# Kernel tuning notes

Measured on AMD Instinct MI355X. Metric: run time of the kernel, lower is better.

The kernel has to match this reference:

```python
import jax, jax.numpy as jnp
import numpy as np

B, T, C = 8, 1024, 768
NH = 12
HD = C // NH  # 64


def setup_inputs() -> dict:
    key = jax.random.key(0)
    k1, k2, k3 = jax.random.split(key, 3)
    x = jax.random.normal(k1, (B, T, C), dtype=jnp.float32)
    w_attn = jax.random.normal(k2, (C, 3 * C), dtype=jnp.float32) * 0.02
    b_attn = jnp.zeros((3 * C,), dtype=jnp.float32)
    w_proj = jax.random.normal(k3, (C, C), dtype=jnp.float32) * 0.02
    b_proj = jnp.zeros((C,), dtype=jnp.float32)
    return {"x": x, "w_attn": w_attn, "b_attn": b_attn, "w_proj": w_proj, "b_proj": b_proj}


def reference(x, w_attn, b_attn, w_proj, b_proj):
    Bb, Tt, Cc = x.shape
    qkv = x @ w_attn + b_attn  # [B,T,3C]
    q, k, v = jnp.split(qkv, [Cc, 2 * Cc], axis=-1)
    # [B, NH, T, HD]
    q = q.reshape(Bb, Tt, NH, HD).swapaxes(1, 2)
    k = k.reshape(Bb, Tt, NH, HD).swapaxes(1, 2)
    v = v.reshape(Bb, Tt, NH, HD).swapaxes(1, 2)
    scale = 1.0 / jnp.sqrt(jnp.asarray(HD, dtype=x.dtype))
    att = jnp.einsum("bhqd,bhkd->bhqk", q, k) * scale  # [B,NH,T,T]
    causal = jnp.tril(jnp.ones((Tt, Tt), dtype=bool))[None, None]
    att = jnp.where(causal, att, jnp.asarray(-jnp.inf, dtype=att.dtype))
    att = jax.nn.softmax(att, axis=-1)
    y = jnp.einsum("bhqk,bhkd->bhqd", att, v)  # [B,NH,T,HD]
    y = y.swapaxes(1, 2).reshape(Bb, Tt, Cc)
    return y @ w_proj + b_proj
```

## Files before the change

kernel.cpp:

```cpp
#include <hip/hip_runtime.h>
#include <cstdint>
#include <cstddef>

typedef __attribute__((ext_vector_type(8))) short short8;
typedef __attribute__((ext_vector_type(4))) float f32x4;
typedef __attribute__((ext_vector_type(4))) unsigned short u16x4;

#define ASYNC16(gp, lp) \
  __builtin_amdgcn_global_load_lds((const __attribute__((address_space(1))) unsigned int*)(gp), \
                                   (__attribute__((address_space(3))) unsigned int*)(lp), 16, 0, 0)

__device__ __forceinline__ unsigned short f2b(float f) {
  union { float f; unsigned int u; } c; c.f = f;
  unsigned int u = c.u;
  return (unsigned short)((u + 0x7fffu + ((u >> 16) & 1u)) >> 16);
}


__global__ __launch_bounds__(256) void prep(
    const float* __restrict__ x, unsigned short* __restrict__ xb,
    const float* __restrict__ w_attn, unsigned short* __restrict__ waT,
    const float* __restrict__ w_proj, unsigned short* __restrict__ wpT) {
  __shared__ unsigned short Ts[64][65];
  const int bb = blockIdx.x;
  const int tid = threadIdx.x;
  if (bb < 3072) {
    int i = (bb * 256 + tid) * 8;
    const float* px = x + i;
    short8 v;
    for (int e = 0; e < 8; ++e) ((unsigned short*)&v)[e] = f2b(px[e]);
    *(short8*)(xb + i) = v;
    return;
  }
  const float* W; unsigned short* WT; int Kd, Nd, n0, k0;
  if (bb < 3504) {
    int t = bb - 3072; W = w_attn; WT = waT; Kd = 768; Nd = 2304;
    n0 = (t % 36) * 64; k0 = (t / 36) * 64;
  } else {
    int t = bb - 3504; W = w_proj; WT = wpT; Kd = 768; Nd = 768;
    n0 = (t % 12) * 64; k0 = (t / 12) * 64;
  }
  for (int idx = tid; idx < 4096; idx += 256) {
    int lr = idx >> 6, lc = idx & 63;
    Ts[lr][lc] = f2b(W[(size_t)(k0 + lr) * Nd + n0 + lc]);
  }
  __syncthreads();
  for (int idx = tid; idx < 4096; idx += 256) {
    int nr = idx >> 6, kc = idx & 63;
    WT[(size_t)(n0 + nr) * Kd + k0 + kc] = Ts[kc][nr];
  }
}


__global__ __launch_bounds__(256, 4) void gemm_qkv(
    const unsigned short* __restrict__ A,
    const unsigned short* __restrict__ Bt,
    const float* __restrict__ bias,
    unsigned short* __restrict__ q,
    unsigned short* __restrict__ k,
    unsigned short* __restrict__ vT)
{
  __shared__ unsigned short As[2][128 * 32];
  __shared__ unsigned short Bs[2][128 * 32];
  const int tid = threadIdx.x;
  const int w = tid >> 6, lane = tid & 63;
  const int wm = w >> 1, wn = w & 1;
  const int lr = lane & 15, lq = lane >> 4;
  const int m0 = blockIdx.x * 128, n0 = blockIdx.y * 128;
  const f32x4 fzero = {0.f, 0.f, 0.f, 0.f};

  f32x4 acc[4][4];
  for (int i = 0; i < 4; ++i) for (int j = 0; j < 4; ++j) acc[i][j] = fzero;

  for (int kk0 = 0; kk0 < 768; kk0 += 64) {
    __syncthreads();
    for (int ks = 0; ks < 2; ++ks)
      for (int c = 0; c < 2; ++c) {
        int base = (c * 4 + w) * 1024;
        int e = (base >> 1) + lane * 8;
        int row = e >> 5, kc = e & 31;
        ASYNC16(A  + (size_t)(m0 + row) * 768 + kk0 + ks * 32 + kc, (char*)As[ks] + base);
        ASYNC16(Bt + (size_t)(n0 + row) * 768 + kk0 + ks * 32 + kc, (char*)Bs[ks] + base);
      }
    __builtin_amdgcn_s_waitcnt(0);
    __syncthreads();

    for (int ks = 0; ks < 2; ++ks) {
      short8 a[4], b[4];
      for (int i = 0; i < 4; ++i)
        a[i] = *(const short8*)(As[ks] + (wm * 64 + i * 16 + lr) * 32 + lq * 8);
      for (int j = 0; j < 4; ++j)
        b[j] = *(const short8*)(Bs[ks] + (wn * 64 + j * 16 + lr) * 32 + lq * 8);
      for (int i = 0; i < 4; ++i)
        for (int j = 0; j < 4; ++j)
          acc[i][j] = __builtin_amdgcn_mfma_f32_16x16x32_bf16(a[i], b[j], acc[i][j], 0, 0, 0);
    }
  }

  const int colbase = n0 + wn * 64;
  const int sec = colbase / 768;
  const float QSCALE = 0.18033688011112042f;
  for (int j = 0; j < 4; ++j) {
    int col = colbase + j * 16 + lr;
    int cc = col - sec * 768;
    int h = cc >> 6, d = cc & 63;
    float bv = bias[col];
    for (int i = 0; i < 4; ++i) {
      int row0 = m0 + wm * 64 + i * 16 + lq * 4;
      int bidx = row0 >> 10, t0 = row0 & 1023;
      int bh = bidx * 12 + h;
      if (sec == 0) {
        for (int r = 0; r < 4; ++r)
          q[((size_t)bh * 1024 + t0 + r) * 64 + d] = f2b((acc[i][j][r] + bv) * QSCALE);
      } else if (sec == 1) {
        for (int r = 0; r < 4; ++r)
          k[((size_t)bh * 1024 + t0 + r) * 64 + d] = f2b(acc[i][j][r] + bv);
      } else {
        u16x4 pv;
        pv[0] = f2b(acc[i][j][0] + bv);
        pv[1] = f2b(acc[i][j][1] + bv);
        pv[2] = f2b(acc[i][j][2] + bv);
        pv[3] = f2b(acc[i][j][3] + bv);
        *(u16x4*)(vT + ((size_t)bh * 64 + d) * 1024 + t0) = pv;
      }
    }
  }
}


__global__ __launch_bounds__(256, 3) void attn(
    const unsigned short* __restrict__ q,
    const unsigned short* __restrict__ kk,
    const unsigned short* __restrict__ vT,
    unsigned short* __restrict__ y)
{
  __shared__ unsigned short Qs[128 * 72];
  __shared__ unsigned short Ks[64 * 72];
  __shared__ unsigned short Vt[64 * 72];
  __shared__ unsigned short Ps[4 * 16 * 72];

  const int tid = threadIdx.x;
  const int w = tid >> 6, lane = tid & 63;
  const int lr = lane & 15, lq = lane >> 4;
  const int g = blockIdx.x;
  const int bh = g % 96;
  const int qp = g / 96;
  const int qt1 = 15 - qp;
  const int b = bh / 12, h = bh - b * 12;
  const f32x4 fzero = {0.f, 0.f, 0.f, 0.f};

  unsigned short* Pw = Ps + w * 16 * 72;
  const unsigned short* kbase = kk + (size_t)bh * 65536;
  const unsigned short* vbase = vT + (size_t)bh * 65536;

  {
    const unsigned short* qa = q + ((size_t)bh * 1024 + qp * 64) * 64;
    const unsigned short* qb = q + ((size_t)bh * 1024 + qt1 * 64) * 64;
    for (int c = tid; c < 512; c += 256) {
      int row = c >> 3, d0 = (c & 7) * 8;
      *(short8*)(Qs + row * 72 + d0)        = *(const short8*)(qa + (size_t)c * 8);
      *(short8*)(Qs + (row + 64) * 72 + d0) = *(const short8*)(qb + (size_t)c * 8);
    }
  }

  const int c0 = tid, c1 = tid + 256;
  short8 kreg[2], vreg[2];
  kreg[0] = *(const short8*)(kbase + (size_t)c0 * 8);
  kreg[1] = *(const short8*)(kbase + (size_t)c1 * 8);
  vreg[0] = *(const short8*)(vbase + (size_t)(c0 >> 3) * 1024 + (c0 & 7) * 8);
  vreg[1] = *(const short8*)(vbase + (size_t)(c1 >> 3) * 1024 + (c1 & 7) * 8);

  f32x4 o0[4], o1[4];
  float l0[4], l1[4];
  for (int jd = 0; jd < 4; ++jd) { o0[jd] = fzero; o1[jd] = fzero; }
  for (int r = 0; r < 4; ++r) { l0[r] = 0.0f; l1[r] = 0.0f; }

  const int nkt = qt1 + 1;

  for (int kt = 0; kt < nkt; ++kt) {
    __syncthreads();
    *(short8*)(Ks + (c0 >> 3) * 72 + (c0 & 7) * 8) = kreg[0];
    *(short8*)(Ks + (c1 >> 3) * 72 + (c1 & 7) * 8) = kreg[1];
    *(short8*)(Vt + (c0 >> 3) * 72 + (c0 & 7) * 8) = vreg[0];
    *(short8*)(Vt + (c1 >> 3) * 72 + (c1 & 7) * 8) = vreg[1];
    __syncthreads();
    if (kt + 1 < nkt) {
      const unsigned short* kp = kbase + (size_t)(kt + 1) * 4096;
      const unsigned short* vp = vbase + (size_t)(kt + 1) * 64;
      kreg[0] = *(const short8*)(kp + (size_t)c0 * 8);
      kreg[1] = *(const short8*)(kp + (size_t)c1 * 8);
      vreg[0] = *(const short8*)(vp + (size_t)(c0 >> 3) * 1024 + (c0 & 7) * 8);
      vreg[1] = *(const short8*)(vp + (size_t)(c1 >> 3) * 1024 + (c1 & 7) * 8);
    }

    short8 bk[2][4];
    for (int ks = 0; ks < 2; ++ks)
      for (int j = 0; j < 4; ++j)
        bk[ks][j] = *(const short8*)(Ks + (j * 16 + lr) * 72 + ks * 32 + lq * 8);

    if (kt <= qp) {
      f32x4 s[4];
      for (int j = 0; j < 4; ++j) s[j] = fzero;
      for (int ks = 0; ks < 2; ++ks) {
        short8 aq = *(const short8*)(Qs + (w * 16 + lr) * 72 + ks * 32 + lq * 8);
        for (int j = 0; j < 4; ++j)
          s[j] = __builtin_amdgcn_mfma_f32_16x16x32_bf16(aq, bk[ks][j], s[j], 0, 0, 0);
      }
      if (kt == qp) {
        int rowt = w * 16 + lq * 4;
        for (int j = 0; j < 4; ++j) {
          int colt = j * 16 + lr;
          for (int r = 0; r < 4; ++r)
            if (colt > rowt + r) s[j][r] = -1e30f;
        }
      }
      for (int r = 0; r < 4; ++r) {
        int prow = (lq * 4 + r) * 72;
        float acc = 0.0f;
        for (int j = 0; j < 4; ++j) {
          float p = __builtin_amdgcn_exp2f(s[j][r]);
          acc += p;
          union { float f; unsigned int u; } cv; cv.f = p;
          Pw[prow + j * 16 + lr] = (unsigned short)((cv.u + 0x8000u) >> 16);
        }
        l0[r] += acc;
      }
      for (int ks = 0; ks < 2; ++ks) {
        short8 ap = *(const short8*)(Pw + lr * 72 + ks * 32 + lq * 8);
        short8 bv[4];
        for (int jd = 0; jd < 4; ++jd)
          bv[jd] = *(const short8*)(Vt + (jd * 16 + lr) * 72 + ks * 32 + lq * 8);
        for (int jd = 0; jd < 4; ++jd)
          o0[jd] = __builtin_amdgcn_mfma_f32_16x16x32_bf16(ap, bv[jd], o0[jd], 0, 0, 0);
      }
    }

    {
      f32x4 s[4];
      for (int j = 0; j < 4; ++j) s[j] = fzero;
      for (int ks = 0; ks < 2; ++ks) {
        short8 aq = *(const short8*)(Qs + (64 + w * 16 + lr) * 72 + ks * 32 + lq * 8);
        for (int j = 0; j < 4; ++j)
          s[j] = __builtin_amdgcn_mfma_f32_16x16x32_bf16(aq, bk[ks][j], s[j], 0, 0, 0);
      }
      if (kt == qt1) {
        int rowt = w * 16 + lq * 4;
        for (int j = 0; j < 4; ++j) {
          int colt = j * 16 + lr;
          for (int r = 0; r < 4; ++r)
            if (colt > rowt + r) s[j][r] = -1e30f;
        }
      }
      for (int r = 0; r < 4; ++r) {
        int prow = (lq * 4 + r) * 72;
        float acc = 0.0f;
        for (int j = 0; j < 4; ++j) {
          float p = __builtin_amdgcn_exp2f(s[j][r]);
          acc += p;
          union { float f; unsigned int u; } cv; cv.f = p;
          Pw[prow + j * 16 + lr] = (unsigned short)((cv.u + 0x8000u) >> 16);
        }
        l1[r] += acc;
      }
      for (int ks = 0; ks < 2; ++ks) {
        short8 ap = *(const short8*)(Pw + lr * 72 + ks * 32 + lq * 8);
        short8 bv[4];
        for (int jd = 0; jd < 4; ++jd)
          bv[jd] = *(const short8*)(Vt + (jd * 16 + lr) * 72 + ks * 32 + lq * 8);
        for (int jd = 0; jd < 4; ++jd)
          o1[jd] = __builtin_amdgcn_mfma_f32_16x16x32_bf16(ap, bv[jd], o1[jd], 0, 0, 0);
      }
    }
  }

  for (int r = 0; r < 4; ++r) {
    float a0 = l0[r], a1 = l1[r];
    for (int off = 1; off < 16; off <<= 1) {
      a0 += __shfl_xor(a0, off, 16);
      a1 += __shfl_xor(a1, off, 16);
    }
    l0[r] = 1.0f / a0;
    l1[r] = 1.0f / a1;
  }
  int t0 = qp * 64 + w * 16 + lq * 4;
  int t1 = qt1 * 64 + w * 16 + lq * 4;
  for (int jd = 0; jd < 4; ++jd) {
    int d = jd * 16 + lr;
    for (int r = 0; r < 4; ++r) {
      y[((size_t)b * 1024 + t0 + r) * 768 + h * 64 + d] = f2b(o0[jd][r] * l0[r]);
      y[((size_t)b * 1024 + t1 + r) * 768 + h * 64 + d] = f2b(o1[jd][r] * l1[r]);
    }
  }
}


__global__ __launch_bounds__(256, 4) void gemm_proj(
    const unsigned short* __restrict__ A,
    const unsigned short* __restrict__ Bt,
    const float* __restrict__ bias,
    float* __restrict__ out)
{
  __shared__ unsigned short As[2][64 * 32];
  __shared__ unsigned short Bs[2][128 * 32];
  const int tid = threadIdx.x;
  const int w = tid >> 6, lane = tid & 63;
  const int wm = w >> 1, wn = w & 1;
  const int lr = lane & 15, lq = lane >> 4;
  const int m0 = blockIdx.x * 64, n0 = blockIdx.y * 128;
  const f32x4 fzero = {0.f, 0.f, 0.f, 0.f};

  f32x4 acc[2][4];
  for (int i = 0; i < 2; ++i) for (int j = 0; j < 4; ++j) acc[i][j] = fzero;

  const int ea = (w * 1024 >> 1) + lane * 8;
  const int arow = ea >> 5, akc = ea & 31;

  for (int kk0 = 0; kk0 < 768; kk0 += 64) {
    __syncthreads();
    for (int ks = 0; ks < 2; ++ks) {
      ASYNC16(A + (size_t)(m0 + arow) * 768 + kk0 + ks * 32 + akc, (char*)As[ks] + w * 1024);
      for (int c = 0; c < 2; ++c) {
        int base = (c * 4 + w) * 1024;
        int e = (base >> 1) + lane * 8;
        int row = e >> 5, kc = e & 31;
        ASYNC16(Bt + (size_t)(n0 + row) * 768 + kk0 + ks * 32 + kc, (char*)Bs[ks] + base);
      }
    }
    __builtin_amdgcn_s_waitcnt(0);
    __syncthreads();

    for (int ks = 0; ks < 2; ++ks) {
      short8 a[2], b[4];
      for (int i = 0; i < 2; ++i)
        a[i] = *(const short8*)(As[ks] + (wm * 32 + i * 16 + lr) * 32 + lq * 8);
      for (int j = 0; j < 4; ++j)
        b[j] = *(const short8*)(Bs[ks] + (wn * 64 + j * 16 + lr) * 32 + lq * 8);
      for (int i = 0; i < 2; ++i)
        for (int j = 0; j < 4; ++j)
          acc[i][j] = __builtin_amdgcn_mfma_f32_16x16x32_bf16(a[i], b[j], acc[i][j], 0, 0, 0);
    }
  }

  for (int j = 0; j < 4; ++j) {
    int col = n0 + wn * 64 + j * 16 + lr;
    float bv = bias[col];
    for (int i = 0; i < 2; ++i) {
      int row0 = m0 + wm * 32 + i * 16 + lq * 4;
      for (int r = 0; r < 4; ++r)
        out[(size_t)(row0 + r) * 768 + col] = acc[i][j][r] + bv;
    }
  }
}


extern "C" void kernel_launch(void* const* d_in, const int* in_sizes, int n_in,
                              void* d_out, int out_size, void* d_ws, size_t ws_size,
                              hipStream_t stream) {
  const float* x      = (const float*)d_in[0];
  const float* w_attn = (const float*)d_in[1];
  const float* b_attn = (const float*)d_in[2];
  const float* w_proj = (const float*)d_in[3];
  const float* b_proj = (const float*)d_in[4];
  float* out = (float*)d_out;

  char* p = (char*)d_ws;
  unsigned short* xb  = (unsigned short*)p; p += (size_t)8192 * 768 * 2;
  unsigned short* waT = (unsigned short*)p; p += (size_t)2304 * 768 * 2;
  unsigned short* wpT = (unsigned short*)p; p += (size_t)768 * 768 * 2;
  unsigned short* qb  = (unsigned short*)p; p += (size_t)96 * 1024 * 64 * 2;
  unsigned short* kb  = (unsigned short*)p; p += (size_t)96 * 1024 * 64 * 2;
  unsigned short* vTb = (unsigned short*)p; p += (size_t)96 * 64 * 1024 * 2;
  unsigned short* yb  = (unsigned short*)p; p += (size_t)8192 * 768 * 2;

  prep<<<3648, 256, 0, stream>>>(x, xb, w_attn, waT, w_proj, wpT);
  gemm_qkv<<<dim3(64, 18), 256, 0, stream>>>(xb, waT, b_attn, qb, kb, vTb);
  attn<<<768, 256, 0, stream>>>(qb, kb, vTb, yb);
  gemm_proj<<<dim3(128, 6), 256, 0, stream>>>(yb, wpT, b_proj, out);
}
```

Measured before the change: 184.4 us.

## Triple-buffer QKV and projection GEMM K-loops with async LDS prefetch

```diff
diff --git a/kernel.cpp b/kernel.cpp
--- a/kernel.cpp
+++ b/kernel.cpp
@@ -52,7 +52,7 @@
 }
 
 
-__global__ __launch_bounds__(256, 4) void gemm_qkv(
+__global__ __launch_bounds__(256, 3) void gemm_qkv(
     const unsigned short* __restrict__ A,
     const unsigned short* __restrict__ Bt,
     const float* __restrict__ bias,
@@ -60,8 +60,8 @@
     unsigned short* __restrict__ k,
     unsigned short* __restrict__ vT)
 {
-  __shared__ unsigned short As[2][128 * 32];
-  __shared__ unsigned short Bs[2][128 * 32];
+  __shared__ unsigned short As[3][128 * 32];
+  __shared__ unsigned short Bs[3][128 * 32];
   const int tid = threadIdx.x;
   const int w = tid >> 6, lane = tid & 63;
   const int wm = w >> 1, wn = w & 1;
@@ -72,30 +72,48 @@
   f32x4 acc[4][4];
   for (int i = 0; i < 4; ++i) for (int j = 0; j < 4; ++j) acc[i][j] = fzero;
 
-  for (int kk0 = 0; kk0 < 768; kk0 += 64) {
-    __syncthreads();
-    for (int ks = 0; ks < 2; ++ks)
-      for (int c = 0; c < 2; ++c) {
-        int base = (c * 4 + w) * 1024;
-        int e = (base >> 1) + lane * 8;
-        int row = e >> 5, kc = e & 31;
-        ASYNC16(A  + (size_t)(m0 + row) * 768 + kk0 + ks * 32 + kc, (char*)As[ks] + base);
-        ASYNC16(Bt + (size_t)(n0 + row) * 768 + kk0 + ks * 32 + kc, (char*)Bs[ks] + base);
-      }
-    __builtin_amdgcn_s_waitcnt(0);
-    __syncthreads();
-
-    for (int ks = 0; ks < 2; ++ks) {
-      short8 a[4], b[4];
-      for (int i = 0; i < 4; ++i)
-        a[i] = *(const short8*)(As[ks] + (wm * 64 + i * 16 + lr) * 32 + lq * 8);
+  const int b0 = w * 1024, b1 = 4096 + w * 1024;
+  const int e0 = (b0 >> 1) + lane * 8, e1 = (b1 >> 1) + lane * 8;
+  const int r0 = e0 >> 5, c0 = e0 & 31, r1 = e1 >> 5, c1 = e1 & 31;
+  const unsigned short* Arow0 = A + (size_t)(m0 + r0) * 768 + c0;
+  const unsigned short* Arow1 = A + (size_t)(m0 + r1) * 768 + c1;
+  const unsigned short* Brow0 = Bt + (size_t)(n0 + r0) * 768 + c0;
+  const unsigned short* Brow1 = Bt + (size_t)(n0 + r1) * 768 + c1;
+
+#define STAGE_QKV(s, bidx) do { \
+    const int kq_ = (s) * 32; \
+    ASYNC16(Arow0 + kq_, (char*)As[bidx] + b0); \
+    ASYNC16(Arow1 + kq_, (char*)As[bidx] + b1); \
+    ASYNC16(Brow0 + kq_, (char*)Bs[bidx] + b0); \
+    ASYNC16(Brow1 + kq_, (char*)Bs[bidx] + b1); \
+  } while (0)
+
+  STAGE_QKV(0, 0);
+  STAGE_QKV(1, 1);
+
+  int bi = 0;
+  for (int s = 0; s < 24; ++s) {
+    if (s < 23) asm volatile("s_waitcnt vmcnt(4)" ::: "memory");
+    else        asm volatile("s_waitcnt vmcnt(0)" ::: "memory");
+    __builtin_amdgcn_s_barrier();
+    __builtin_amdgcn_sched_barrier(0);
+    if (s + 2 < 24) {
+      int b2 = bi + 2; if (b2 >= 3) b2 -= 3;
+      STAGE_QKV(s + 2, b2);
+    }
+    const unsigned short* asb = As[bi];
+    const unsigned short* bsb = Bs[bi];
+    short8 a[4], b[4];
+    for (int i = 0; i < 4; ++i)
+      a[i] = *(const short8*)(asb + (wm * 64 + i * 16 + lr) * 32 + lq * 8);
+    for (int j = 0; j < 4; ++j)
+      b[j] = *(const short8*)(bsb + (wn * 64 + j * 16 + lr) * 32 + lq * 8);
+    for (int i = 0; i < 4; ++i)
       for (int j = 0; j < 4; ++j)
-        b[j] = *(const short8*)(Bs[ks] + (wn * 64 + j * 16 + lr) * 32 + lq * 8);
-      for (int i = 0; i < 4; ++i)
-        for (int j = 0; j < 4; ++j)
-          acc[i][j] = __builtin_amdgcn_mfma_f32_16x16x32_bf16(a[i], b[j], acc[i][j], 0, 0, 0);
-    }
-  }
+        acc[i][j] = __builtin_amdgcn_mfma_f32_16x16x32_bf16(a[i], b[j], acc[i][j], 0, 0, 0);
+    ++bi; if (bi == 3) bi = 0;
+  }
+#undef STAGE_QKV
 
   const int colbase = n0 + wn * 64;
   const int sec = colbase / 768;
@@ -300,8 +318,8 @@
     const float* __restrict__ bias,
     float* __restrict__ out)
 {
-  __shared__ unsigned short As[2][64 * 32];
-  __shared__ unsigned short Bs[2][128 * 32];
+  __shared__ unsigned short As[3][64 * 32];
+  __shared__ unsigned short Bs[3][128 * 32];
   const int tid = threadIdx.x;
   const int w = tid >> 6, lane = tid & 63;
   const int wm = w >> 1, wn = w & 1;
@@ -312,34 +330,49 @@
   f32x4 acc[2][4];
   for (int i = 0; i < 2; ++i) for (int j = 0; j < 4; ++j) acc[i][j] = fzero;
 
-  const int ea = (w * 1024 >> 1) + lane * 8;
-  const int arow = ea >> 5, akc = ea & 31;
-
-  for (int kk0 = 0; kk0 < 768; kk0 += 64) {
-    __syncthreads();
-    for (int ks = 0; ks < 2; ++ks) {
-      ASYNC16(A + (size_t)(m0 + arow) * 768 + kk0 + ks * 32 + akc, (char*)As[ks] + w * 1024);
-      for (int c = 0; c < 2; ++c) {
-        int base = (c * 4 + w) * 1024;
-        int e = (base >> 1) + lane * 8;
-        int row = e >> 5, kc = e & 31;
-        ASYNC16(Bt + (size_t)(n0 + row) * 768 + kk0 + ks * 32 + kc, (char*)Bs[ks] + base);
-      }
-    }
-    __builtin_amdgcn_s_waitcnt(0);
-    __syncthreads();
-
-    for (int ks = 0; ks < 2; ++ks) {
-      short8 a[2], b[4];
-      for (int i = 0; i < 2; ++i)
-        a[i] = *(const short8*)(As[ks] + (wm * 32 + i * 16 + lr) * 32 + lq * 8);
+  const int ba = w * 1024;
+  const int ea = (ba >> 1) + lane * 8;
+  const int ar = ea >> 5, ac = ea & 31;
+  const int b0 = w * 1024, b1 = 4096 + w * 1024;
+  const int e0 = (b0 >> 1) + lane * 8, e1 = (b1 >> 1) + lane * 8;
+  const int r0 = e0 >> 5, c0 = e0 & 31, r1 = e1 >> 5, c1 = e1 & 31;
+  const unsigned short* Arow  = A + (size_t)(m0 + ar) * 768 + ac;
+  const unsigned short* Brow0 = Bt + (size_t)(n0 + r0) * 768 + c0;
+  const unsigned short* Brow1 = Bt + (size_t)(n0 + r1) * 768 + c1;
+
+#define STAGE_PROJ(s, bidx) do { \
+    const int kq_ = (s) * 32; \
+    ASYNC16(Arow  + kq_, (char*)As[bidx] + ba); \
+    ASYNC16(Brow0 + kq_, (char*)Bs[bidx] + b0); \
+    ASYNC16(Brow1 + kq_, (char*)Bs[bidx] + b1); \
+  } while (0)
+
+  STAGE_PROJ(0, 0);
+  STAGE_PROJ(1, 1);
+
+  int bi = 0;
+  for (int s = 0; s < 24; ++s) {
+    if (s < 23) asm volatile("s_waitcnt vmcnt(3)" ::: "memory");
+    else        asm volatile("s_waitcnt vmcnt(0)" ::: "memory");
+    __builtin_amdgcn_s_barrier();
+    __builtin_amdgcn_sched_barrier(0);
+    if (s + 2 < 24) {
+      int b2 = bi + 2; if (b2 >= 3) b2 -= 3;
+      STAGE_PROJ(s + 2, b2);
+    }
+    const unsigned short* asb = As[bi];
+    const unsigned short* bsb = Bs[bi];
+    short8 a[2], b[4];
+    for (int i = 0; i < 2; ++i)
+      a[i] = *(const short8*)(asb + (wm * 32 + i * 16 + lr) * 32 + lq * 8);
+    for (int j = 0; j < 4; ++j)
+      b[j] = *(const short8*)(bsb + (wn * 64 + j * 16 + lr) * 32 + lq * 8);
+    for (int i = 0; i < 2; ++i)
       for (int j = 0; j < 4; ++j)
-        b[j] = *(const short8*)(Bs[ks] + (wn * 64 + j * 16 + lr) * 32 + lq * 8);
-      for (int i = 0; i < 2; ++i)
-        for (int j = 0; j < 4; ++j)
-          acc[i][j] = __builtin_amdgcn_mfma_f32_16x16x32_bf16(a[i], b[j], acc[i][j], 0, 0, 0);
-    }
-  }
+        acc[i][j] = __builtin_amdgcn_mfma_f32_16x16x32_bf16(a[i], b[j], acc[i][j], 0, 0, 0);
+    ++bi; if (bi == 3) bi = 0;
+  }
+#undef STAGE_PROJ
 
   for (int j = 0; j < 4; ++j) {
     int col = n0 + wn * 64 + j * 16 + lr;
```

Measured after the change: 188.0 us. About the same (+2.0%).
